# Kernel tuning notes

Measured on AMD Instinct MI355X. Metric: run time of the kernel, lower is better.

The kernel has to match this reference:

```python
import jax, jax.numpy as jnp
import numpy as np

N_IN = 1024
N_OUT = 2048
EMBED_DIM = 1024  # == n_in so multi-layer path type-checks
LAYERS = 2
T, B = 128, 64


def setup_inputs() -> dict:
    key = jax.random.key(0)
    ks = jax.random.split(key, 8)
    s_in = 1.0 / np.sqrt(N_IN)
    s_out = 1.0 / np.sqrt(N_OUT)
    return {
        "xt": jax.random.normal(ks[0], (T, B, N_IN), jnp.float32),
        "ct_forward": jnp.zeros((LAYERS, B, N_OUT), jnp.float32),
        # weights stored [in, out] (transposed vs torch Linear)
        "Wx": jax.random.uniform(ks[1], (N_IN, N_OUT), jnp.float32, -s_in, s_in),
        "Wf": jax.random.uniform(ks[2], (N_IN, N_OUT), jnp.float32, -s_in, s_in),
        "bf": jnp.zeros((N_OUT,), jnp.float32),
        "Wr": jax.random.uniform(ks[3], (N_IN, N_OUT), jnp.float32, -s_in, s_in),
        "br": jnp.zeros((N_OUT,), jnp.float32),
        "Wcx": jax.random.uniform(ks[4], (N_IN, N_OUT), jnp.float32, -s_in, s_in),
        "bcx": jnp.zeros((N_OUT,), jnp.float32),
        "Wcl": jax.random.uniform(ks[5], (N_OUT, EMBED_DIM), jnp.float32, -s_out, s_out),
        "bcl": jnp.zeros((EMBED_DIM,), jnp.float32),
    }


def _one_layer(x, c0, Wx, Wf, bf, Wr, br, Wcx, bcx):
    # x: [T, B, n_in]; c0: [B, n_out]
    # batch all projections over time (compute-dense GEMMs)
    xp = jnp.einsum("tbi,io->tbo", x, Wx)                     # x_t projection
    f = jax.nn.sigmoid(jnp.einsum("tbi,io->tbo", x, Wf) + bf)  # forget gate
    r = jax.nn.sigmoid(jnp.einsum("tbi,io->tbo", x, Wr) + br)  # reset gate
    cx = jnp.einsum("tbi,io->tbo", x, Wcx) + bcx               # highway path

    def step(c, inp):
        f_t, xp_t = inp
        c_new = f_t * c + (1.0 - f_t) * xp_t
        return c_new, c_new

    c_last, c_seq = jax.lax.scan(step, c0, (f, xp))
    h = r * jnp.tanh(c_seq) + (1.0 - r) * cx
    return h, c_last


def reference(xt, ct_forward, Wx, Wf, bf, Wr, br, Wcx, bcx, Wcl, bcl):
    x = xt
    c_last = ct_forward[0]
    for l in range(LAYERS):
        if x.shape[2] == N_OUT:  # layers >= 2: project back to embed_dim (= n_in)
            x = jnp.einsum("tbo,oe->tbe", x, Wcl) + bcl
        x, c_last = _one_layer(x, ct_forward[l], Wx, Wf, bf, Wr, br, Wcx, bcx)
    # dropout p=0.0 -> identity
    return x, c_last
```

## Files before the change

kernel.cpp:

```cpp
#include <hip/hip_runtime.h>

#define TT 128
#define BB 64
#define NIN 1024
#define NOUT 2048
#define MR (TT*BB)

typedef unsigned short u16;
typedef __attribute__((ext_vector_type(8))) __bf16 bf16x8;
typedef __attribute__((ext_vector_type(4))) float f32x4;
typedef __attribute__((ext_vector_type(8))) unsigned short u16x8;

static __device__ __forceinline__ u16 f2bf(float f) {
    union { float f; unsigned u; } v; v.f = f;
    unsigned r = v.u + 0x7fffu + ((v.u >> 16) & 1u);
    return (u16)(r >> 16);
}
static __device__ __forceinline__ float bf2f(u16 x) {
    union { unsigned u; float f; } v; v.u = ((unsigned)x) << 16;
    return v.f;
}

__global__ void k_cvt_chunk(const float* __restrict__ s, u16* __restrict__ d, int M_, int K_) {
    __shared__ float t[64][33];
    int m0 = blockIdx.x * 64, k0 = blockIdx.y * 32;
    int ml = threadIdx.x >> 3, kl = (threadIdx.x & 7) * 4;
    #pragma unroll
    for (int p = 0; p < 2; ++p) {
        float4 v = *(const float4*)&s[(size_t)(m0 + ml + p * 32) * K_ + k0 + kl];
        t[ml + p * 32][kl] = v.x; t[ml + p * 32][kl + 1] = v.y;
        t[ml + p * 32][kl + 2] = v.z; t[ml + p * 32][kl + 3] = v.w;
    }
    __syncthreads();
    int q = threadIdx.x >> 6, row = threadIdx.x & 63;
    u16x8 o;
    #pragma unroll
    for (int j = 0; j < 8; ++j) o[j] = f2bf(t[row][q * 8 + j]);
    *(u16x8*)&d[(((size_t)(k0 >> 3) + q) * M_ + m0 + row) * 8] = o;
}

__global__ void k_wT_chunk(const float* __restrict__ s, u16* __restrict__ d,
                           int K_, int N_, int OUTM, int row_off) {
    __shared__ float t[32][65];
    int k0 = blockIdx.y * 32, n0 = blockIdx.x * 64;
    int kl = threadIdx.x >> 6, nl = threadIdx.x & 63;
    #pragma unroll
    for (int p = 0; p < 8; ++p)
        t[kl + p * 4][nl] = s[(size_t)(k0 + kl + p * 4) * N_ + n0 + nl];
    __syncthreads();
    int q = threadIdx.x >> 6, row = threadIdx.x & 63;
    u16x8 o;
    #pragma unroll
    for (int j = 0; j < 8; ++j) o[j] = f2bf(t[q * 8 + j][row]);
    *(u16x8*)&d[(((size_t)(k0 >> 3) + q) * OUTM + row_off + n0 + row) * 8] = o;
}

__global__ void k_bias_pack(const float* __restrict__ bf_, const float* __restrict__ br_,
                            const float* __restrict__ bcx_, float* __restrict__ ball) {
    int i = blockIdx.x * 256 + threadIdx.x;
    int g = i >> 11, n = i & 2047;
    float v = 0.f;
    if (g == 1) v = bf_[n];
    else if (g == 2) v = br_[n];
    else if (g == 3) v = bcx_[n];
    ball[i] = v;
}

#define GLL16(SRC, DST) __builtin_amdgcn_global_load_lds( \
    (const __attribute__((address_space(1))) void*)(SRC), \
    (__attribute__((address_space(3))) void*)(DST), 16, 0, 0)
#define SBAR() __builtin_amdgcn_s_barrier()
#define SCHED0() __builtin_amdgcn_sched_barrier(0)
#define VM8 asm volatile("s_waitcnt vmcnt(8)" ::: "memory")
#define VM4 asm volatile("s_waitcnt vmcnt(4)" ::: "memory")
#define VM3 asm volatile("s_waitcnt vmcnt(3)" ::: "memory")
#define VM0 asm volatile("s_waitcnt vmcnt(0)" ::: "memory")

__global__ __launch_bounds__(512, 2) void k_gemm8(
    const u16* __restrict__ A, const u16* __restrict__ BT,
    const float* __restrict__ bias, u16* __restrict__ outG,
    int M, int NB, int K)
{
    constexpr int BUF = 16384;
    __shared__ __align__(16) u16 L[4 * BUF];

    const int tid = threadIdx.x;
    const int w = tid >> 6, lane = tid & 63;
    const int wr = w >> 2, wc = w & 3;
    const int lr = lane & 15, kq = lane >> 4;
    const int flat = blockIdx.y * gridDim.x + blockIdx.x;
    const int xcd = flat & 7, bi = flat >> 3;
    const int n0 = (xcd * 4 + (bi & 3)) * 256;
    const int m0 = (bi >> 2) * 256;
    const int nk = K >> 5;

    const int t1 = tid + 512;
    const u16* aS0 = A + ((size_t)(tid >> 8) * M + m0 + (tid & 255)) * 8;
    const u16* aS1 = A + ((size_t)(t1 >> 8) * M + m0 + (t1 & 255)) * 8;
    const u16* bS0 = BT + ((size_t)(tid >> 8) * NB + n0 + (tid & 255)) * 8;
    const u16* bS1 = BT + ((size_t)(t1 >> 8) * NB + n0 + (t1 & 255)) * 8;
    const int aD0 = (w * 64) * 8, aD1 = (512 + w * 64) * 8;
    const int bD0 = 8192 + aD0, bD1 = 8192 + aD1;
    const size_t aStep = (size_t)32 * M, bStep = (size_t)32 * NB;

    const int rA0 = (kq * 256 + wr * 128 + lr) * 8;
    const int rA1 = (kq * 256 + wr * 128 + 64 + lr) * 8;
    const int rB  = (kq * 256 + wc * 64 + lr) * 8;

    f32x4 acc[8][4] = {};
    bf16x8 aF0[4], aF1[4], bF0[4], bF1[4];

#define STAGE(TAU) { const size_t _oA = (size_t)(TAU) * aStep, _oB = (size_t)(TAU) * bStep; \
    const int _wb = ((TAU) & 3) * BUF; \
    GLL16(aS0 + _oA, &L[_wb + aD0]); GLL16(aS1 + _oA, &L[_wb + aD1]); \
    GLL16(bS0 + _oB, &L[_wb + bD0]); GLL16(bS1 + _oB, &L[_wb + bD1]); }
#define LDAP(DST, BB_) { _Pragma("unroll") for (int i = 0; i < 4; ++i) \
    DST[i] = *(const bf16x8*)&L[(BB_) + rA0 + i * 128]; }
#define LDAG(DST, BB_) { _Pragma("unroll") for (int i = 0; i < 4; ++i) \
    DST[i] = *(const bf16x8*)&L[(BB_) + rA1 + i * 128]; }
#define LDBP(DST, BB_) { _Pragma("unroll") for (int j = 0; j < 4; ++j) \
    DST[j] = *(const bf16x8*)&L[(BB_) + 8192 + rB + j * 128]; }
#define MM0(BF) { _Pragma("unroll") for (int i = 0; i < 4; ++i) \
    _Pragma("unroll") for (int j = 0; j < 4; ++j) \
        acc[i][j] = __builtin_amdgcn_mfma_f32_16x16x32_bf16(aF0[i], BF[j], acc[i][j], 0, 0, 0); }
#define MM4(BF) { _Pragma("unroll") for (int i = 0; i < 4; ++i) \
    _Pragma("unroll") for (int j = 0; j < 4; ++j) \
        acc[i + 4][j] = __builtin_amdgcn_mfma_f32_16x16x32_bf16(aF1[i], BF[j], acc[i + 4][j], 0, 0, 0); }

#define ITER(T_, BC, BN_) { \
    const int t_ = (T_); \
    const bool st3 = (t_ + 3) < nk, st2 = (t_ + 2) < nk; \
    const int tn = (t_ + 1 < nk) ? t_ + 1 : nk - 1; \
    const int cb = (t_ & 3) * BUF, nb = (tn & 3) * BUF; \
     \
    if (st3) STAGE(t_ + 3); \
    LDAG(aF1, cb); \
    if (st3) { VM8; } else if (st2) { VM4; } else { VM0; } \
    SBAR(); \
    __builtin_amdgcn_s_setprio(1); MM0(bF##BC); __builtin_amdgcn_s_setprio(0); \
    SBAR(); \
     \
    LDAP(aF0, nb); LDBP(bF##BN_, nb); \
    SBAR(); \
    __builtin_amdgcn_s_setprio(1); MM4(bF##BC); __builtin_amdgcn_s_setprio(0); \
    SBAR(); SCHED0(); }

    STAGE(0); STAGE(1); STAGE(2);
    VM8; SBAR();
    LDAP(aF0, 0); LDBP(bF0, 0);

    for (int t2 = 0; t2 < nk; t2 += 2) {
        ITER(t2 + 0, 0, 1);
        ITER(t2 + 1, 1, 0);
    }
#undef ITER
#undef STAGE
#undef LDAP
#undef LDAG
#undef LDBP
#undef MM0
#undef MM4

    const size_t GM2 = (size_t)M << 11;
    #pragma unroll
    for (int i = 0; i < 8; ++i) {
        int r0 = m0 + wr * 128 + i * 16 + kq * 4;
        #pragma unroll
        for (int j = 0; j < 4; ++j) {
            int gc = n0 + wc * 64 + j * 16 + lr;
            float bv = bias[gc];
            int g = gc >> 11;
            bool sig = (g == 1 || g == 2);
            size_t base = (size_t)g * GM2 + (size_t)(gc & 2047);
            #pragma unroll
            for (int q = 0; q < 4; ++q) {
                float v = acc[i][j][q] + bv;
                if (sig) v = 1.f / (1.f + __expf(-v));
                outG[base + (size_t)(r0 + q) * 2048] = f2bf(v);
            }
        }
    }
}

__global__ __launch_bounds__(512, 2) void k_gemm4(
    const u16* __restrict__ A, const u16* __restrict__ BT,
    const float* __restrict__ bias, u16* __restrict__ outC,
    int M, int NB, int K)
{
    constexpr int BM = 128;
    constexpr int BUF = BM * 32 + 8192;
    __shared__ __align__(16) u16 L[4 * BUF];

    const int tid = threadIdx.x;
    const int w = tid >> 6, lane = tid & 63;
    const int wr = w >> 2, wc = w & 3;
    const int lr = lane & 15, kq = lane >> 4;
    const int gx = gridDim.x;
    const int nwg = gx * gridDim.y;
    const int flat = blockIdx.y * gx + blockIdx.x;
    const int swz = (flat & 7) * (nwg >> 3) + (flat >> 3);
    const int m0 = (swz / gx) * BM, n0 = (swz % gx) * 256;
    const int nk = K >> 5;

    const u16* aSrc1; int aDst1;
    {
        int q = tid >> 7, row = tid & 127;
        aSrc1 = A + ((size_t)q * M + m0 + row) * 8;
        aDst1 = (w * 64) * 8;
    }
    const u16* bSrc[2]; int bDst[2];
    #pragma unroll
    for (int l = 0; l < 2; ++l) {
        int tc = tid + l * 512;
        bSrc[l] = BT + ((size_t)(tc >> 8) * NB + n0 + (tc & 255)) * 8;
        bDst[l] = BM * 32 + (w * 64 + l * 512) * 8;
    }
    const size_t aStep = (size_t)32 * M;
    const size_t bStep = (size_t)32 * NB;
    const int rdA = wr * 64 + lr;
    const int rdB = wc * 64 + lr;

    f32x4 acc[4][4] = {};
    bf16x8 aP0[4], bP0[4], aP1[4], bP1[4];

    #pragma unroll
    for (int p = 0; p < 3; ++p) {
        GLL16(aSrc1 + (size_t)p * aStep, &L[p * BUF + aDst1]);
        #pragma unroll
        for (int l = 0; l < 2; ++l) GLL16(bSrc[l] + (size_t)p * bStep, &L[p * BUF + bDst[l]]);
    }
    VM3;
    SBAR(); SCHED0();
    #pragma unroll
    for (int i = 0; i < 4; ++i) aP0[i] = *(const bf16x8*)&L[(kq * BM + rdA + i * 16) * 8];
    #pragma unroll
    for (int j = 0; j < 4; ++j) bP0[j] = *(const bf16x8*)&L[BM * 32 + (kq * 256 + rdB + j * 16) * 8];

#define ITER4(KT, CUR, NXT) { \
    const int kt_ = (KT); \
    const int tn = (kt_ + 1 < nk) ? kt_ + 1 : nk - 1; \
    const int nb = (tn & 3) * BUF; \
    if (kt_ + 3 < nk) { \
        const size_t sa = (size_t)(kt_ + 3) * aStep, sb_ = (size_t)(kt_ + 3) * bStep; \
        const int wb = ((kt_ + 3) & 3) * BUF; \
        GLL16(aSrc1 + sa, &L[wb + aDst1]); \
        _Pragma("unroll") for (int l = 0; l < 2; ++l) GLL16(bSrc[l] + sb_, &L[wb + bDst[l]]); \
    } \
    __builtin_amdgcn_s_setprio(1); \
    _Pragma("unroll") for (int i = 0; i < 4; ++i) \
        _Pragma("unroll") for (int j = 0; j < 4; ++j) \
            acc[i][j] = __builtin_amdgcn_mfma_f32_16x16x32_bf16(aP##CUR[i], bP##CUR[j], acc[i][j], 0, 0, 0); \
    _Pragma("unroll") for (int i = 0; i < 4; ++i) \
        aP##NXT[i] = *(const bf16x8*)&L[nb + (kq * BM + rdA + i * 16) * 8]; \
    _Pragma("unroll") for (int j = 0; j < 4; ++j) \
        bP##NXT[j] = *(const bf16x8*)&L[nb + BM * 32 + (kq * 256 + rdB + j * 16) * 8]; \
    __builtin_amdgcn_s_setprio(0); \
    if (kt_ + 3 < nk) { VM3; } else { VM0; } \
    SBAR(); SCHED0(); }

    for (int kt4 = 0; kt4 < nk; kt4 += 4) {
        ITER4(kt4 + 0, 0, 1);
        ITER4(kt4 + 1, 1, 0);
        ITER4(kt4 + 2, 0, 1);
        ITER4(kt4 + 3, 1, 0);
    }
#undef ITER4

    #pragma unroll
    for (int i = 0; i < 4; ++i) {
        int r0 = m0 + wr * 64 + i * 16 + kq * 4;
        #pragma unroll
        for (int j = 0; j < 4; ++j) {
            int gc = n0 + wc * 64 + j * 16 + lr;
            float bv = bias[gc];
            size_t base = ((size_t)(gc >> 3) * M) * 8 + (size_t)(gc & 7);
            #pragma unroll
            for (int q = 0; q < 4; ++q)
                outC[base + (size_t)(r0 + q) * 8] = f2bf(acc[i][j][q] + bv);
        }
    }
}

__global__ void k_scan(const u16* __restrict__ G, const float* __restrict__ c0,
                       u16* __restrict__ hb, float* __restrict__ hf,
                       float* __restrict__ cout)
{
    int idx = blockIdx.x * 256 + threadIdx.x;
    int b = idx >> 11, n = idx & 2047;
    float c = c0[idx];
    const size_t GM = (size_t)MR * 2048;
    const size_t hcBase = ((size_t)(n >> 3) * MR) * 8 + (size_t)(n & 7);
    for (int t = 0; t < TT; ++t) {
        int m = t * BB + b;
        size_t p = ((size_t)m << 11) + (size_t)n;
        float xp = bf2f(G[p]);
        float f  = bf2f(G[GM + p]);
        float r  = bf2f(G[2 * GM + p]);
        float cx = bf2f(G[3 * GM + p]);
        c = f * c + (1.f - f) * xp;
        float h = r * tanhf(c) + (1.f - r) * cx;
        if (hb) hb[hcBase + (size_t)m * 8] = f2bf(h);
        if (hf) hf[p] = h;
    }
    if (cout) cout[idx] = c;
}

extern "C" void kernel_launch(void* const* d_in, const int* in_sizes, int n_in,
                              void* d_out, int out_size, void* d_ws, size_t ws_size,
                              hipStream_t stream)
{
    const float* xt  = (const float*)d_in[0];
    const float* ctf = (const float*)d_in[1];
    const float* Wx  = (const float*)d_in[2];
    const float* Wf  = (const float*)d_in[3];
    const float* bfp = (const float*)d_in[4];
    const float* Wr  = (const float*)d_in[5];
    const float* brp = (const float*)d_in[6];
    const float* Wcx = (const float*)d_in[7];
    const float* bcx = (const float*)d_in[8];
    const float* Wcl = (const float*)d_in[9];
    const float* bcl = (const float*)d_in[10];
    float* out = (float*)d_out;

    char* ws = (char*)d_ws;
    u16* x0 = (u16*)ws;       ws += (size_t)MR * NIN * 2;
    u16* x2 = (u16*)ws;       ws += (size_t)MR * NIN * 2;
    u16* h1 = (u16*)ws;       ws += (size_t)MR * NOUT * 2;
    u16* WTall = (u16*)ws;    ws += (size_t)4 * NOUT * NIN * 2;
    u16* WclT = (u16*)ws;     ws += (size_t)NIN * NOUT * 2;
    float* ball = (float*)ws; ws += (size_t)4 * NOUT * 4;
    u16* G = (u16*)ws;        ws += (size_t)4 * MR * NOUT * 2;

    k_cvt_chunk<<<dim3(MR / 64, NIN / 32), 256, 0, stream>>>(xt, x0, MR, NIN);
    k_wT_chunk<<<dim3(NOUT / 64, NIN / 32), 256, 0, stream>>>(Wx,  WTall, NIN, NOUT, 4 * NOUT, 0 * NOUT);
    k_wT_chunk<<<dim3(NOUT / 64, NIN / 32), 256, 0, stream>>>(Wf,  WTall, NIN, NOUT, 4 * NOUT, 1 * NOUT);
    k_wT_chunk<<<dim3(NOUT / 64, NIN / 32), 256, 0, stream>>>(Wr,  WTall, NIN, NOUT, 4 * NOUT, 2 * NOUT);
    k_wT_chunk<<<dim3(NOUT / 64, NIN / 32), 256, 0, stream>>>(Wcx, WTall, NIN, NOUT, 4 * NOUT, 3 * NOUT);
    k_wT_chunk<<<dim3(NIN / 64, NOUT / 32), 256, 0, stream>>>(Wcl, WclT, NOUT, NIN, NIN, 0);
    k_bias_pack<<<32, 256, 0, stream>>>(bfp, brp, bcx, ball);

    k_gemm8<<<dim3(32, 32), 512, 0, stream>>>(x0, WTall, ball, G, MR, 4 * NOUT, NIN);
    k_scan<<<(BB * NOUT) / 256, 256, 0, stream>>>(G, ctf, h1, (float*)nullptr, (float*)nullptr);

    k_gemm4<<<dim3(NIN / 256, MR / 128), 512, 0, stream>>>(h1, WclT, bcl, x2, MR, NIN, NOUT);

    k_gemm8<<<dim3(32, 32), 512, 0, stream>>>(x2, WTall, ball, G, MR, 4 * NOUT, NIN);
    k_scan<<<(BB * NOUT) / 256, 256, 0, stream>>>(G, ctf + (size_t)BB * NOUT, (u16*)nullptr, out, out + (size_t)MR * NOUT);
}
```

Baseline: 503.9 us.

## Restructure GEMM main loop to one barrier per two K-steps

Replaces the per-K-step pipeline (three stages in flight, four barriers per step, fine-grained vmcnt waits) with a loop that handles two K-steps per iteration. Global-to-LDS prefetch runs only two stages ahead, and each iteration ends with a single full vmcnt(0) wait plus one barrier. The intent is to cut barrier and synchronisation overhead and give the scheduler longer MFMA runs. The occupancy hint of two blocks per CU is dropped from launch_bounds. In exchange the full drain each iteration exposes more global-load latency, and the register budget changes.

```diff
diff --git a/kernel.cpp b/kernel.cpp
--- a/kernel.cpp
+++ b/kernel.cpp
@@ -71,12 +71,10 @@
     (__attribute__((address_space(3))) void*)(DST), 16, 0, 0)
 #define SBAR() __builtin_amdgcn_s_barrier()
 #define SCHED0() __builtin_amdgcn_sched_barrier(0)
-#define VM8 asm volatile("s_waitcnt vmcnt(8)" ::: "memory")
-#define VM4 asm volatile("s_waitcnt vmcnt(4)" ::: "memory")
 #define VM3 asm volatile("s_waitcnt vmcnt(3)" ::: "memory")
 #define VM0 asm volatile("s_waitcnt vmcnt(0)" ::: "memory")
 
-__global__ __launch_bounds__(512, 2) void k_gemm8(
+__global__ __launch_bounds__(512) void k_gemm8(
     const u16* __restrict__ A, const u16* __restrict__ BT,
     const float* __restrict__ bias, u16* __restrict__ outG,
     int M, int NB, int K)
@@ -108,7 +106,7 @@
     const int rB  = (kq * 256 + wc * 64 + lr) * 8;
 
     f32x4 acc[8][4] = {};
-    bf16x8 aF0[4], aF1[4], bF0[4], bF1[4];
+    bf16x8 aP0[4], bP0[4], aP1[4], bP1[4];
 
 #define STAGE(TAU) { const size_t _oA = (size_t)(TAU) * aStep, _oB = (size_t)(TAU) * bStep; \
     const int _wb = ((TAU) & 3) * BUF; \
@@ -120,46 +118,51 @@
     DST[i] = *(const bf16x8*)&L[(BB_) + rA1 + i * 128]; }
 #define LDBP(DST, BB_) { _Pragma("unroll") for (int j = 0; j < 4; ++j) \
     DST[j] = *(const bf16x8*)&L[(BB_) + 8192 + rB + j * 128]; }
-#define MM0(BF) { _Pragma("unroll") for (int i = 0; i < 4; ++i) \
+#define MML(AF, BF) { _Pragma("unroll") for (int i = 0; i < 4; ++i) \
     _Pragma("unroll") for (int j = 0; j < 4; ++j) \
-        acc[i][j] = __builtin_amdgcn_mfma_f32_16x16x32_bf16(aF0[i], BF[j], acc[i][j], 0, 0, 0); }
-#define MM4(BF) { _Pragma("unroll") for (int i = 0; i < 4; ++i) \
+        acc[i][j] = __builtin_amdgcn_mfma_f32_16x16x32_bf16(AF[i], BF[j], acc[i][j], 0, 0, 0); }
+#define MMU(AF, BF) { _Pragma("unroll") for (int i = 0; i < 4; ++i) \
     _Pragma("unroll") for (int j = 0; j < 4; ++j) \
-        acc[i + 4][j] = __builtin_amdgcn_mfma_f32_16x16x32_bf16(aF1[i], BF[j], acc[i + 4][j], 0, 0, 0); }
-
-#define ITER(T_, BC, BN_) { \
-    const int t_ = (T_); \
-    const bool st3 = (t_ + 3) < nk, st2 = (t_ + 2) < nk; \
-    const int tn = (t_ + 1 < nk) ? t_ + 1 : nk - 1; \
-    const int cb = (t_ & 3) * BUF, nb = (tn & 3) * BUF; \
-     \
-    if (st3) STAGE(t_ + 3); \
-    LDAG(aF1, cb); \
-    if (st3) { VM8; } else if (st2) { VM4; } else { VM0; } \
-    SBAR(); \
-    __builtin_amdgcn_s_setprio(1); MM0(bF##BC); __builtin_amdgcn_s_setprio(0); \
-    SBAR(); \
-     \
-    LDAP(aF0, nb); LDBP(bF##BN_, nb); \
-    SBAR(); \
-    __builtin_amdgcn_s_setprio(1); MM4(bF##BC); __builtin_amdgcn_s_setprio(0); \
-    SBAR(); SCHED0(); }
-
-    STAGE(0); STAGE(1); STAGE(2);
-    VM8; SBAR();
-    LDAP(aF0, 0); LDBP(bF0, 0);
-
-    for (int t2 = 0; t2 < nk; t2 += 2) {
-        ITER(t2 + 0, 0, 1);
-        ITER(t2 + 1, 1, 0);
-    }
-#undef ITER
+        acc[i + 4][j] = __builtin_amdgcn_mfma_f32_16x16x32_bf16(AF[i], BF[j], acc[i + 4][j], 0, 0, 0); }
+
+    STAGE(0); STAGE(1);
+    VM0; SBAR(); SCHED0();
+    LDAP(aP0, 0); LDBP(bP0, 0);
+
+    for (int t = 0; t < nk; t += 2) {
+        const int cb = (t & 3) * BUF;
+        const int nb = ((t + 1) & 3) * BUF;
+        const bool s2 = (t + 2) < nk, s3 = (t + 3) < nk;
+        {
+            bf16x8 aG[4];
+            LDAG(aG, cb);
+            if (s2) STAGE(t + 2);
+            __builtin_amdgcn_s_setprio(1);
+            MML(aP0, bP0);
+            __builtin_amdgcn_s_setprio(0);
+            LDAP(aP1, nb); LDBP(bP1, nb);
+            __builtin_amdgcn_s_setprio(1);
+            MMU(aG, bP0);
+            __builtin_amdgcn_s_setprio(0);
+        }
+        {
+            bf16x8 aG[4];
+            LDAG(aG, nb);
+            if (s3) STAGE(t + 3);
+            __builtin_amdgcn_s_setprio(1);
+            MML(aP1, bP1);
+            MMU(aG, bP1);
+            __builtin_amdgcn_s_setprio(0);
+        }
+        VM0; SBAR(); SCHED0();
+        if (s2) { LDAP(aP0, ((t + 2) & 3) * BUF); LDBP(bP0, ((t + 2) & 3) * BUF); }
+    }
 #undef STAGE
 #undef LDAP
 #undef LDAG
 #undef LDBP
-#undef MM0
-#undef MM4
+#undef MML
+#undef MMU
 
     const size_t GM2 = (size_t)M << 11;
     #pragma unroll
```

After: 471.8 us. 1.07x faster.
